# Kernel tuning notes

Measured on AMD Instinct MI355X. Metric: run time of the kernel, lower is better.

The kernel has to match this reference:

```python
import jax, jax.numpy as jnp
import numpy as np

N_NODES = 100000

def gcn_conv(x, W, b, src, dst, n):
    # PyG GCNConv: h = x @ W; add self-loops; norm = D^-1/2 (A+I) D^-1/2; aggregate at dst.
    h = x @ W  # [N, out]
    deg = jnp.zeros((n,), h.dtype).at[dst].add(1.0) + 1.0  # +1 for self-loop
    d = jax.lax.rsqrt(deg)  # deg >= 1 always
    norm = d[src] * d[dst]  # [E]
    agg = jnp.zeros_like(h).at[dst].add(norm[:, None] * h[src])  # scatter-add neighbor messages
    agg = agg + h * (d * d)[:, None]  # self-loop contribution (norm = d_i^2)
    return agg + b


def setup_inputs() -> dict:
    key = jax.random.key(0)
    k1, k2, k3, k4 = jax.random.split(key, 4)
    F_in, H, C = 128, 64, 16
    E = 3200000
    x = jax.random.normal(k1, (N_NODES, F_in), dtype=jnp.float32)
    edges = jax.random.randint(k2, (E, 2), 0, N_NODES, dtype=jnp.int64)
    # Glorot-style init for weights, zero bias (as in GCNConv.reset_parameters)
    W1 = jax.random.normal(k3, (F_in, H), dtype=jnp.float32) * (1.0 / np.sqrt(F_in))
    b1 = jnp.zeros((H,), jnp.float32)
    W2 = jax.random.normal(k4, (H, C), dtype=jnp.float32) * (1.0 / np.sqrt(H))
    b2 = jnp.zeros((C,), jnp.float32)
    return {"x": x, "edges": edges, "W1": W1, "b1": b1, "W2": W2, "b2": b2}


def reference(x, edges, W1, b1, W2, b2):
    src, dst = edges[:, 0], edges[:, 1]
    h = jax.nn.relu(gcn_conv(x, W1, b1, src, dst, N_NODES))
    out = gcn_conv(h, W2, b2, src, dst, N_NODES)
    return out
```

## Files before the change

### kernel.cpp

```cpp
#include <hip/hip_runtime.h>

#define N_NODES 100000
#define F_IN    128
#define H_DIM   64
#define C_DIM   16
#define NBKT    391
#define BKT_PAD 16
#define CHUNK   8192
#define CAP     8960

typedef __attribute__((ext_vector_type(8))) short bf16x8;
typedef __attribute__((ext_vector_type(4))) float f32x4;

__device__ __forceinline__ void fma4(float4& acc, float s, const float4& w) {
    acc.x = fmaf(s, w.x, acc.x);
    acc.y = fmaf(s, w.y, acc.y);
    acc.z = fmaf(s, w.z, acc.z);
    acc.w = fmaf(s, w.w, acc.w);
}
__device__ __forceinline__ unsigned bfr(float f) {
    unsigned u = __float_as_uint(f);
    return (u + (((u >> 16) & 1u) + 0x7FFFu)) >> 16;
}
__device__ __forceinline__ void accb(float4& a, uint2 u) {
    a.x += __uint_as_float(u.x << 16);
    a.y += __uint_as_float(u.x & 0xFFFF0000u);
    a.z += __uint_as_float(u.y << 16);
    a.w += __uint_as_float(u.y & 0xFFFF0000u);
}

__global__ __launch_bounds__(512) void k_bfill(const int2* __restrict__ edges,
                                               int* __restrict__ bkt_tail,
                                               int* __restrict__ pairs, int E) {
    __shared__ int2 sp[CHUNK];
    __shared__ int  cnt[NBKT];
    __shared__ int  lbase[NBKT];
    __shared__ int  row[NBKT];
    __shared__ int  scn[512];
    int t = threadIdx.x;
    for (int i = t; i < NBKT; i += 512) cnt[i] = 0;
    __syncthreads();
    int base = blockIdx.x * CHUNK;
    int m    = min(E - base, CHUNK);
    int2 ed[16];
    int  rk[16];
    #pragma unroll
    for (int i = 0; i < 16; ++i) {
        int e = i * 512 + t;
        if (e < m) {
            ed[i] = edges[base + e];
            rk[i] = atomicAdd(&cnt[ed[i].y >> 8], 1);
        }
    }
    __syncthreads();
    scn[t] = (t < NBKT) ? cnt[t] : 0;
    __syncthreads();
    #pragma unroll
    for (int off = 1; off < 512; off <<= 1) {
        int v = (t >= off) ? scn[t - off] : 0;
        __syncthreads();
        scn[t] += v;
        __syncthreads();
    }
    for (int b = t; b < NBKT; b += 512) {
        int c = cnt[b];
        lbase[b] = scn[b] - c;
        row[b]   = c ? atomicAdd(&bkt_tail[b * BKT_PAD], c) : 0;
    }
    __syncthreads();
    #pragma unroll
    for (int i = 0; i < 16; ++i) {
        int e = i * 512 + t;
        if (e < m) sp[lbase[ed[i].y >> 8] + rk[i]] = ed[i];
    }
    __syncthreads();
    #pragma unroll
    for (int i = 0; i < 16; ++i) {
        int idx = i * 512 + t;
        if (idx < m) {
            int2 p   = sp[idx];
            int  bkt = p.y >> 8;
            int  wpos = row[bkt] + (idx - lbase[bkt]);
            if (wpos < CAP) pairs[bkt * CAP + wpos] = (p.x << 8) | (p.y & 255);
        }
    }
}

__global__ __launch_bounds__(1024) void k_bnode(const int* __restrict__ pairs,
                                                const int* __restrict__ bkt_tail,
                                                int* __restrict__ csr_src,
                                                int* __restrict__ node_base,
                                                int* __restrict__ node_cnt,
                                                float* __restrict__ dinv) {
    __shared__ int sc[CAP];
    __shared__ int cnt[256];
    __shared__ int row[256];
    __shared__ int wsum[4];
    int b = blockIdx.x;
    int t = threadIdx.x;
    if (t < 256) cnt[t] = 0;
    __syncthreads();
    int start = b * CAP;
    int m     = min(bkt_tail[b * BKT_PAD], CAP);
    for (int e = t; e < m; e += 1024)
        atomicAdd(&cnt[pairs[start + e] & 255], 1);
    __syncthreads();
    if (t < 256) {
        int c = cnt[t];
        int lane = t & 63, wv = t >> 6;
        int v = c;
        #pragma unroll
        for (int off = 1; off < 64; off <<= 1) {
            int u = __shfl_up(v, off);
            if (lane >= off) v += u;
        }
        if (lane == 63) wsum[wv] = v;
        __syncthreads();
        int woff = 0;
        #pragma unroll
        for (int w = 0; w < 4; ++w) woff += (w < wv) ? wsum[w] : 0;
        int incl = v + woff;
        row[t] = incl - c;
        int node = b * 256 + t;
        if (node < N_NODES) {
            node_base[node] = start + incl - c;
            node_cnt[node]  = c;
            dinv[node]      = rsqrtf((float)(c + 1));
        }
    } else {
        __syncthreads();
    }
    __syncthreads();
    for (int e = t; e < m; e += 1024) {
        int p   = pairs[start + e];
        int pos = atomicAdd(&row[p & 255], 1);
        sc[pos] = ((unsigned)p) >> 8;
    }
    __syncthreads();
    for (int e = t; e < m; e += 1024)
        csr_src[start + e] = sc[e];
}

__global__ __launch_bounds__(256) void k_gemm1(const float* __restrict__ x,
                                               const float* __restrict__ W1,
                                               const float* __restrict__ dinv,
                                               uint2* __restrict__ g1b) {
    __shared__ short wt[64][132];
    int tid = threadIdx.x;
    {
        int n  = tid & 63;
        int k0 = (tid >> 6) * 32;
        #pragma unroll 8
        for (int k = 0; k < 32; ++k)
            wt[n][k0 + k] = (short)bfr(W1[(size_t)(k0 + k) * H_DIM + n]);
    }
    __syncthreads();

    int wave = tid >> 6, lane = tid & 63;
    int tile = blockIdx.x * 4 + wave;
    bool valid = tile < N_NODES / 16;
    int row0 = (valid ? tile : 0) * 16;
    int l15  = lane & 15;
    int kg   = lane >> 4;
    const float* xrow = x + (size_t)(row0 + l15) * F_IN;

    f32x4 ac0 = {0.f,0.f,0.f,0.f}, ac1 = ac0, ac2 = ac0, ac3 = ac0;
    #pragma unroll
    for (int ks = 0; ks < 4; ++ks) {
        int kb = ks * 32 + kg * 8;
        float4 p0 = *(const float4*)(xrow + kb);
        float4 p1 = *(const float4*)(xrow + kb + 4);
        bf16x8 a;
        a[0] = (short)bfr(p0.x); a[1] = (short)bfr(p0.y);
        a[2] = (short)bfr(p0.z); a[3] = (short)bfr(p0.w);
        a[4] = (short)bfr(p1.x); a[5] = (short)bfr(p1.y);
        a[6] = (short)bfr(p1.z); a[7] = (short)bfr(p1.w);
        bf16x8 b0 = *(const bf16x8*)&wt[l15     ][kb];
        bf16x8 b1 = *(const bf16x8*)&wt[l15 + 16][kb];
        bf16x8 b2 = *(const bf16x8*)&wt[l15 + 32][kb];
        bf16x8 b3 = *(const bf16x8*)&wt[l15 + 48][kb];
        ac0 = __builtin_amdgcn_mfma_f32_16x16x32_bf16(a, b0, ac0, 0, 0, 0);
        ac1 = __builtin_amdgcn_mfma_f32_16x16x32_bf16(a, b1, ac1, 0, 0, 0);
        ac2 = __builtin_amdgcn_mfma_f32_16x16x32_bf16(a, b2, ac2, 0, 0, 0);
        ac3 = __builtin_amdgcn_mfma_f32_16x16x32_bf16(a, b3, ac3, 0, 0, 0);
    }
    if (!valid) return;

    int rbase = row0 + kg * 4;
    #pragma unroll
    for (int r = 0; r < 4; ++r) {
        float di = dinv[rbase + r];
        size_t gro = (size_t)(rbase + r) * 16;
        #pragma unroll
        for (int ct = 0; ct < 4; ++ct) {
            float v = ((ct == 0) ? ac0[r] : (ct == 1) ? ac1[r] :
                       (ct == 2) ? ac2[r] : ac3[r]) * di;
            float v1 = __shfl_down(v, 1);
            float v2 = __shfl_down(v, 2);
            float v3 = __shfl_down(v, 3);
            if ((l15 & 3) == 0) {
                uint2 pk;
                pk.x = bfr(v)  | (bfr(v1) << 16);
                pk.y = bfr(v2) | (bfr(v3) << 16);
                g1b[gro + ct * 4 + (l15 >> 2)] = pk;
            }
        }
    }
}

__global__ __launch_bounds__(256) void k_gather1(const int* __restrict__ csr_src,
                                                 const int* __restrict__ base,
                                                 const int* __restrict__ cnt,
                                                 const float* __restrict__ dinv,
                                                 const uint2* __restrict__ g1b,
                                                 const float* __restrict__ b1,
                                                 const float* __restrict__ W2,
                                                 uint2* __restrict__ g2b) {
    __shared__ float  w2t[16 * 68];
    __shared__ float4 ysh[4][68];
    int tid = threadIdx.x;
    #pragma unroll
    for (int i = 0; i < 4; ++i) {
        int idx = i * 256 + tid;
        w2t[(idx & 15) * 68 + (idx >> 4)] = W2[idx];
    }
    __syncthreads();

    int lane = tid & 63;
    int wv   = tid >> 6;
    int grp  = lane >> 4;
    int l16  = lane & 15;
    int g0   = lane & 48;
    int node = ((blockIdx.x * 256 + tid) >> 6) * 4 + grp;
    int   b  = base[node];
    int   c  = cnt[node];
    float di = dinv[node];
    float4 acc = {0.f, 0.f, 0.f, 0.f};
    accb(acc, g1b[(size_t)node * 16 + l16]);

    for (int k0 = 0; k0 < c; k0 += 16) {
        int k = k0 + l16;
        int sidx = (k < c) ? csr_src[b + k] : 0;
        int nj = min(16, c - k0);
        int j = 0;
        for (; j + 4 <= nj; j += 4) {
            int s0 = __shfl(sidx, g0 + j + 0);
            int s1 = __shfl(sidx, g0 + j + 1);
            int s2 = __shfl(sidx, g0 + j + 2);
            int s3 = __shfl(sidx, g0 + j + 3);
            uint2 u0 = g1b[(size_t)s0 * 16 + l16];
            uint2 u1 = g1b[(size_t)s1 * 16 + l16];
            uint2 u2 = g1b[(size_t)s2 * 16 + l16];
            uint2 u3 = g1b[(size_t)s3 * 16 + l16];
            accb(acc, u0); accb(acc, u1); accb(acc, u2); accb(acc, u3);
        }
        for (; j < nj; ++j) {
            accb(acc, g1b[(size_t)__shfl(sidx, g0 + j) * 16 + l16]);
        }
    }

    float4 bv = ((const float4*)b1)[l16];
    float4 y;
    y.x = fmaxf(fmaf(di, acc.x, bv.x), 0.f) * di;
    y.y = fmaxf(fmaf(di, acc.y, bv.y), 0.f) * di;
    y.z = fmaxf(fmaf(di, acc.z, bv.z), 0.f) * di;
    y.w = fmaxf(fmaf(di, acc.w, bv.w), 0.f) * di;
    ysh[wv][grp * 17 + l16] = y;

    float o = 0.f;
    #pragma unroll
    for (int f4 = 0; f4 < 16; ++f4) {
        float4 yv = ysh[wv][grp * 17 + f4];
        const float4* wr = (const float4*)&w2t[l16 * 68 + f4 * 4];
        float4 wv4 = *wr;
        o = fmaf(yv.x, wv4.x, o);
        o = fmaf(yv.y, wv4.y, o);
        o = fmaf(yv.z, wv4.z, o);
        o = fmaf(yv.w, wv4.w, o);
    }
    float o1 = __shfl_down(o, 1);
    float o2 = __shfl_down(o, 2);
    float o3 = __shfl_down(o, 3);
    if ((l16 & 3) == 0) {
        uint2 pk;
        pk.x = bfr(o)  | (bfr(o1) << 16);
        pk.y = bfr(o2) | (bfr(o3) << 16);
        g2b[(size_t)node * 4 + (l16 >> 2)] = pk;
    }
}

__global__ __launch_bounds__(256) void k_gather2(const int* __restrict__ csr_src,
                                                 const int* __restrict__ base,
                                                 const int* __restrict__ cnt,
                                                 const float* __restrict__ dinv,
                                                 const uint2* __restrict__ g2b,
                                                 const float* __restrict__ b2,
                                                 float* __restrict__ out) {
    int tid  = threadIdx.x;
    int lane = tid & 63;
    int grp  = lane >> 2;
    int l4   = lane & 3;
    int g0   = lane & 60;
    int node = ((blockIdx.x * 256 + tid) >> 6) * 16 + grp;
    if (node >= N_NODES) return;
    int   b  = base[node];
    int   c  = cnt[node];
    float di = dinv[node];
    float4 acc = {0.f, 0.f, 0.f, 0.f};
    accb(acc, g2b[(size_t)node * 4 + l4]);

    for (int k0 = 0; k0 < c; k0 += 4) {
        int k = k0 + l4;
        int sidx = (k < c) ? csr_src[b + k] : 0;
        int nj = min(4, c - k0);
        if (nj == 4) {
            int s0 = __shfl(sidx, g0 + 0);
            int s1 = __shfl(sidx, g0 + 1);
            int s2 = __shfl(sidx, g0 + 2);
            int s3 = __shfl(sidx, g0 + 3);
            uint2 u0 = g2b[(size_t)s0 * 4 + l4];
            uint2 u1 = g2b[(size_t)s1 * 4 + l4];
            uint2 u2 = g2b[(size_t)s2 * 4 + l4];
            uint2 u3 = g2b[(size_t)s3 * 4 + l4];
            accb(acc, u0); accb(acc, u1); accb(acc, u2); accb(acc, u3);
        } else {
            for (int j = 0; j < nj; ++j)
                accb(acc, g2b[(size_t)__shfl(sidx, g0 + j) * 4 + l4]);
        }
    }
    float4 bv = ((const float4*)b2)[l4];
    float4 r  = { fmaf(di, acc.x, bv.x), fmaf(di, acc.y, bv.y),
                  fmaf(di, acc.z, bv.z), fmaf(di, acc.w, bv.w) };
    ((float4*)out)[(size_t)node * 4 + l4] = r;
}

extern "C" void kernel_launch(void* const* d_in, const int* in_sizes, int n_in,
                              void* d_out, int out_size, void* d_ws, size_t ws_size,
                              hipStream_t stream) {
    const float* x     = (const float*)d_in[0];
    const int*   edges = (const int*)d_in[1];
    const float* W1    = (const float*)d_in[2];
    const float* b1    = (const float*)d_in[3];
    const float* W2    = (const float*)d_in[4];
    const float* b2    = (const float*)d_in[5];
    float*       out   = (float*)d_out;

    const int E = in_sizes[1] / 2;

    int*   pairs   = (int*)d_ws;
    uint2* g1b     = (uint2*)d_ws;
    uint2* g2b     = (uint2*)((float*)d_ws + (size_t)NBKT * CAP);
    int*   csr_src = (int*)g2b + (size_t)N_NODES * 8 + 64;
    int*   nbase   = csr_src + (size_t)NBKT * CAP;
    int*   ncnt    = nbase + N_NODES;
    float* dinv    = (float*)(ncnt + N_NODES);
    int*   bkt_tail= (int*)(dinv + N_NODES);

    const int nchunk = (E + CHUNK - 1) / CHUNK;

    hipMemsetAsync(bkt_tail, 0, (size_t)NBKT * BKT_PAD * sizeof(int), stream);
    k_bfill  <<<nchunk, 512, 0, stream>>>((const int2*)edges, bkt_tail, pairs, E);
    k_bnode  <<<NBKT, 1024, 0, stream>>>(pairs, bkt_tail, csr_src, nbase, ncnt, dinv);

    k_gemm1   <<<(N_NODES / 16 + 3) / 4, 256, 0, stream>>>(x, W1, dinv, g1b);

    k_gather1 <<<6250, 256, 0, stream>>>(csr_src, nbase, ncnt, dinv, g1b, b1, W2, g2b);

    k_gather2 <<<1563, 256, 0, stream>>>(csr_src, nbase, ncnt, dinv, g2b, b2, out);
}
```

Before: 145.1 us.

## Replace global bucket atomics with per-chunk counts and in-block prefix scan

```diff
diff --git a/kernel.cpp b/kernel.cpp
--- a/kernel.cpp
+++ b/kernel.cpp
@@ -5,19 +5,13 @@
 #define H_DIM   64
 #define C_DIM   16
 #define NBKT    391
-#define BKT_PAD 16
 #define CHUNK   8192
 #define CAP     8960
+#define MAXCH   400
 
 typedef __attribute__((ext_vector_type(8))) short bf16x8;
 typedef __attribute__((ext_vector_type(4))) float f32x4;
 
-__device__ __forceinline__ void fma4(float4& acc, float s, const float4& w) {
-    acc.x = fmaf(s, w.x, acc.x);
-    acc.y = fmaf(s, w.y, acc.y);
-    acc.z = fmaf(s, w.z, acc.z);
-    acc.w = fmaf(s, w.w, acc.w);
-}
 __device__ __forceinline__ unsigned bfr(float f) {
     unsigned u = __float_as_uint(f);
     return (u + (((u >> 16) & 1u) + 0x7FFFu)) >> 16;
@@ -30,12 +24,12 @@
 }
 
 __global__ __launch_bounds__(512) void k_bfill(const int2* __restrict__ edges,
-                                               int* __restrict__ bkt_tail,
-                                               int* __restrict__ pairs, int E) {
+                                               int* __restrict__ pairs_flat,
+                                               int* __restrict__ cnts_g,
+                                               int* __restrict__ lbase_g, int E) {
     __shared__ int2 sp[CHUNK];
     __shared__ int  cnt[NBKT];
     __shared__ int  lbase[NBKT];
-    __shared__ int  row[NBKT];
     __shared__ int  scn[512];
     int t = threadIdx.x;
     for (int i = t; i < NBKT; i += 512) cnt[i] = 0;
@@ -64,8 +58,10 @@
     }
     for (int b = t; b < NBKT; b += 512) {
         int c = cnt[b];
-        lbase[b] = scn[b] - c;
-        row[b]   = c ? atomicAdd(&bkt_tail[b * BKT_PAD], c) : 0;
+        int lb = scn[b] - c;
+        lbase[b] = lb;
+        cnts_g [blockIdx.x * NBKT + b] = c;
+        lbase_g[blockIdx.x * NBKT + b] = lb;
     }
     __syncthreads();
     #pragma unroll
@@ -78,32 +74,59 @@
     for (int i = 0; i < 16; ++i) {
         int idx = i * 512 + t;
         if (idx < m) {
-            int2 p   = sp[idx];
-            int  bkt = p.y >> 8;
-            int  wpos = row[bkt] + (idx - lbase[bkt]);
-            if (wpos < CAP) pairs[bkt * CAP + wpos] = (p.x << 8) | (p.y & 255);
-        }
-    }
-}
-
-__global__ __launch_bounds__(1024) void k_bnode(const int* __restrict__ pairs,
-                                                const int* __restrict__ bkt_tail,
+            int2 p = sp[idx];
+            pairs_flat[base + idx] = (p.x << 8) | (p.y & 255);
+        }
+    }
+}
+
+__global__ __launch_bounds__(1024) void k_bnode(const int* __restrict__ pairs_flat,
+                                                const int* __restrict__ cnts_g,
+                                                const int* __restrict__ lbase_g,
                                                 int* __restrict__ csr_src,
                                                 int* __restrict__ node_base,
                                                 int* __restrict__ node_cnt,
-                                                float* __restrict__ dinv) {
+                                                float* __restrict__ dinv, int nch) {
+    __shared__ int spairs[CAP];
     __shared__ int sc[CAP];
+    __shared__ int roff[MAXCH + 1];
+    __shared__ int rlb[MAXCH];
     __shared__ int cnt[256];
     __shared__ int row[256];
     __shared__ int wsum[4];
+    __shared__ int scn[512];
     int b = blockIdx.x;
     int t = threadIdx.x;
     if (t < 256) cnt[t] = 0;
-    __syncthreads();
-    int start = b * CAP;
-    int m     = min(bkt_tail[b * BKT_PAD], CAP);
-    for (int e = t; e < m; e += 1024)
-        atomicAdd(&cnt[pairs[start + e] & 255], 1);
+    for (int i = t; i < nch; i += 1024) {
+        roff[i] = cnts_g [i * NBKT + b];
+        rlb[i]  = lbase_g[i * NBKT + b];
+    }
+    __syncthreads();
+    if (t < 512) scn[t] = (t < nch) ? roff[t] : 0;
+    __syncthreads();
+    #pragma unroll
+    for (int off = 1; off < 512; off <<= 1) {
+        int v = 0;
+        if (t < 512 && t >= off) v = scn[t - off];
+        __syncthreads();
+        if (t < 512) scn[t] += v;
+        __syncthreads();
+    }
+    if (t < nch) roff[t] = scn[t] - ((t < nch) ? cnts_g[t * NBKT + b] : 0);
+    if (t == 0) roff[nch] = scn[nch - 1];
+    __syncthreads();
+    int m = min(roff[nch], CAP);
+    for (int e = t; e < m; e += 1024) {
+        int lo = 0, hi = nch - 1;
+        while (lo < hi) {
+            int mid = (lo + hi + 1) >> 1;
+            if (roff[mid] <= e) lo = mid; else hi = mid - 1;
+        }
+        int p = pairs_flat[lo * CHUNK + rlb[lo] + (e - roff[lo])];
+        spairs[e] = p;
+        atomicAdd(&cnt[p & 255], 1);
+    }
     __syncthreads();
     if (t < 256) {
         int c = cnt[t];
@@ -123,7 +146,7 @@
         row[t] = incl - c;
         int node = b * 256 + t;
         if (node < N_NODES) {
-            node_base[node] = start + incl - c;
+            node_base[node] = b * CAP + incl - c;
             node_cnt[node]  = c;
             dinv[node]      = rsqrtf((float)(c + 1));
         }
@@ -132,13 +155,13 @@
     }
     __syncthreads();
     for (int e = t; e < m; e += 1024) {
-        int p   = pairs[start + e];
+        int p   = spairs[e];
         int pos = atomicAdd(&row[p & 255], 1);
         sc[pos] = ((unsigned)p) >> 8;
     }
     __syncthreads();
     for (int e = t; e < m; e += 1024)
-        csr_src[start + e] = sc[e];
+        csr_src[b * CAP + e] = sc[e];
 }
 
 __global__ __launch_bounds__(256) void k_gemm1(const float* __restrict__ x,
@@ -345,22 +368,23 @@
     const float* b2    = (const float*)d_in[5];
     float*       out   = (float*)d_out;
 
-    const int E = in_sizes[1] / 2;
-
-    int*   pairs   = (int*)d_ws;
+    const int E   = in_sizes[1] / 2;
+    const int nch = (E + CHUNK - 1) / CHUNK;
+
+    int*   pairs_flat = (int*)d_ws;
     uint2* g1b     = (uint2*)d_ws;
     uint2* g2b     = (uint2*)((float*)d_ws + (size_t)NBKT * CAP);
     int*   csr_src = (int*)g2b + (size_t)N_NODES * 8 + 64;
     int*   nbase   = csr_src + (size_t)NBKT * CAP;
     int*   ncnt    = nbase + N_NODES;
     float* dinv    = (float*)(ncnt + N_NODES);
-    int*   bkt_tail= (int*)(dinv + N_NODES);
-
-    const int nchunk = (E + CHUNK - 1) / CHUNK;
-
-    hipMemsetAsync(bkt_tail, 0, (size_t)NBKT * BKT_PAD * sizeof(int), stream);
-    k_bfill  <<<nchunk, 512, 0, stream>>>((const int2*)edges, bkt_tail, pairs, E);
-    k_bnode  <<<NBKT, 1024, 0, stream>>>(pairs, bkt_tail, csr_src, nbase, ncnt, dinv);
+    int*   cnts_g  = (int*)(dinv + N_NODES);
+    int*   lbase_g = cnts_g + (size_t)nch * NBKT;
+
+    k_bfill <<<nch, 512, 0, stream>>>((const int2*)edges, pairs_flat,
+                                      cnts_g, lbase_g, E);
+    k_bnode <<<NBKT, 1024, 0, stream>>>(pairs_flat, cnts_g, lbase_g, csr_src,
+                                        nbase, ncnt, dinv, nch);
 
     k_gemm1   <<<(N_NODES / 16 + 3) / 4, 256, 0, stream>>>(x, W1, dinv, g1b);
 
```

After: 144.0 us. About the same (-0.8%).
